# Kernel tuning notes

Hardware: AMD Instinct MI355X
Metric: run time of the kernel (lower is better)

Reference implementation:

```python
import jax, jax.numpy as jnp
import numpy as np


def setup_inputs() -> dict:
    key = jax.random.key(0)
    ks = jax.random.split(key, 6)
    B, H, W, Cin, Cout, wdim = 8, 64, 64, 512, 512, 512
    return {
        "x": jax.random.normal(ks[0], (B, H, W, Cin), jnp.float32),
        "w": jax.random.normal(ks[1], (B, wdim), jnp.float32),
        "noise": jax.random.normal(ks[2], (B, H, W, 1), jnp.float32),
        "style_weight": jax.random.normal(ks[3], (wdim, Cin), jnp.float32),
        "style_bias": jnp.ones((Cin,), jnp.float32),
        "conv_weight": jax.random.normal(ks[4], (3, 3, Cin, Cout), jnp.float32),
        "scale_noise": 0.1 * jax.random.normal(ks[5], (1, 1, 1, Cout), jnp.float32),
        "bias": jax.random.normal(jax.random.fold_in(key, 7), (Cout,), jnp.float32),
    }


def reference(x, w, noise, style_weight, style_bias, conv_weight, scale_noise, bias):
    wdim = style_weight.shape[0]
    kh, kw, cin, cout = conv_weight.shape
    # Equalized-LR fully connected to_style (gain=1, lr_mult=1, bias init ones,
    # activation=True -> leaky_relu(0.2) with sqrt(2) gain, StyleGAN2 convention).
    s = w @ (style_weight * (1.0 / np.sqrt(wdim))) + style_bias  # [B, Cin]
    s = jax.nn.leaky_relu(s, 0.2) * np.sqrt(2.0).astype(np.float32)
    # Modulated conv (demodulated). Equalized-LR weight scale 1/sqrt(fan_in).
    wk = conv_weight * (1.0 / np.sqrt(kh * kw * cin))  # [3,3,Cin,Cout]
    # demod[b,o] = rsqrt(sum_{h,w,i} (wk[h,w,i,o]*s[b,i])^2 + eps)
    d = jax.lax.rsqrt(jnp.einsum('hwio,bi->bo', wk * wk, s * s) + 1e-8)  # [B,Cout]
    xm = x * s[:, None, None, :]  # modulate inputs instead of per-sample weights
    y = jax.lax.conv_general_dilated(
        xm, wk, window_strides=(1, 1), padding='SAME',
        dimension_numbers=('NHWC', 'HWIO', 'NHWC'))
    y = y * d[:, None, None, :]
    # noise scale-add + bias + leaky-relu (the fused tail in StyleGAN2 kernels)
    y = y + scale_noise * noise + bias
    return jax.nn.leaky_relu(y, 0.2)
```

## Files before the change

kernel.cpp:

```cpp
#include <hip/hip_runtime.h>
#include <hip/hip_bf16.h>
#include <stdint.h>


typedef __attribute__((ext_vector_type(8))) __bf16 bf16x8;
typedef __attribute__((ext_vector_type(16))) float f32x16;

__device__ __forceinline__ float bf2f(ushort u) {
    union { uint32_t i; float f; } v; v.i = (uint32_t)u << 16; return v.f;
}
__device__ __forceinline__ ushort f2bf(float f) {
    union { float f; uint32_t i; } v; v.f = f;
    uint32_t r = v.i + 0x7fffu + ((v.i >> 16) & 1u);
    return (ushort)(r >> 16);
}
__device__ __forceinline__ int sniff_f32(const void* sb) {
    return ((const uint32_t*)sb)[0] == 0x3F800000u;
}
__device__ __forceinline__ float lda(const void* p, int idx, int isf) {
    return isf ? ((const float*)p)[idx] : bf2f(((const ushort*)p)[idx]);
}

union U16x8 { uint4 v; ushort u[8]; };

#define INV_SQRT_WDIM 0.04419417382415922f
#define SQRT2         1.4142135623730951f
#define WSCALE        0.014731391274719739f

__global__ void k_style_part(const void* __restrict__ w, const void* __restrict__ sw,
                             const void* __restrict__ sb, float* __restrict__ part) {
    int isf = sniff_f32(sb);
    int b = blockIdx.x >> 3, ds = blockIdx.x & 7;
    int i = threadIdx.x;
    __shared__ float wrow[64];
    if (i < 64) wrow[i] = lda(w, b * 512 + ds * 64 + i, isf);
    __syncthreads();
    float acc = 0.f;
    if (isf) {
        const float* p = (const float*)sw + (size_t)ds * 64 * 512;
#pragma unroll 8
        for (int d = 0; d < 64; ++d) acc += wrow[d] * p[d * 512 + i];
    } else {
        const ushort* p = (const ushort*)sw + (size_t)ds * 64 * 512;
#pragma unroll 8
        for (int d = 0; d < 64; ++d) acc += wrow[d] * bf2f(p[d * 512 + i]);
    }
    part[(b * 8 + ds) * 512 + i] = acc;
}

__device__ __forceinline__ float style_s(const float* __restrict__ spart,
                                         const void* __restrict__ sb,
                                         int b, int i, int isf) {
    float a = 0.f;
#pragma unroll
    for (int ds = 0; ds < 8; ++ds) a += spart[(b * 8 + ds) * 512 + i];
    float s = a * INV_SQRT_WDIM + lda(sb, i, isf);
    return (s > 0.f ? s : 0.2f * s) * SQRT2;
}

__global__ void k_prep(const void* __restrict__ cw, const void* __restrict__ x,
                       const float* __restrict__ spart, const void* __restrict__ sb,
                       ushort* __restrict__ wkt2, ushort* __restrict__ xmp2,
                       float* __restrict__ part) {
    int isf = sniff_f32(sb);
    int bid = blockIdx.x;
    int tid = threadIdx.x;
    __shared__ __align__(16) char pool[34816];

    if (bid < 576) {
        ushort (*smw)[512] = (ushort (*)[512])pool;
        int t = bid / 64, ckg = bid % 64;
#pragma unroll
        for (int r = 0; r < 16; ++r) {
            int l = r * 256 + tid;
            int j = l >> 9, o = l & 511;
            float v = lda(cw, (size_t)(t * 512 + ckg * 8 + j) * 512 + o, isf);
            smw[j][o] = f2bf(v * WSCALE);
        }
        __syncthreads();
#pragma unroll
        for (int r = 0; r < 2; ++r) {
            int o = r * 256 + tid;
            U16x8 pk;
#pragma unroll
            for (int j = 0; j < 8; ++j) pk.u[j] = smw[j][o];
            *(uint4*)(wkt2 + ((size_t)(t * 64 + ckg) * 512 + o) * 8) = pk.v;
        }
        return;
    }
    if (bid < 1104) {
        float* sv = (float*)pool;
        ushort* tr = (ushort*)(pool + 2048);
        int pr = bid - 576;
        int b = pr / 66, yp = pr % 66;
        ushort* xb2 = xmp2 + (size_t)b * 2230272;
        uint4 z = {0u, 0u, 0u, 0u};
        if (yp == 0 || yp == 65) {
            for (int l = tid; l < 4224; l += 256) {
                int h = l / 132, cc = l - h * 132;
                *(uint4*)(xb2 + (size_t)(h * 66 + yp) * 1056 + cc * 8) = z;
            }
            return;
        }
        for (int i = tid; i < 512; i += 256) sv[i] = style_s(spart, sb, b, i, isf);
        if (tid < 64) {
            int h = tid & 31, side = tid >> 5;
            ushort* op = xb2 + ((size_t)(h * 66 + yp) * 66 + side * 65) * 16;
            *(uint4*)(op) = z;
            *(uint4*)(op + 8) = z;
        }
        int y = yp - 1;
        __syncthreads();
#pragma unroll 1
        for (int p = 0; p < 2; ++p) {
            if (p) __syncthreads();
            int c0 = p * 32;
#pragma unroll
            for (int r = 0; r < 4; ++r) {
                int u = r * 256 + tid;
                int hg = u & 31, col = u >> 5;
                U16x8 o0_, o1_;
                const float* sp = sv + hg * 16;
                if (isf) {
                    const float* xin = (const float*)x
                        + (((size_t)(b * 64 + y)) * 64 + c0 + col) * 512 + hg * 16;
                    float4 f0 = *(const float4*)(xin + 0);
                    float4 f1 = *(const float4*)(xin + 4);
                    float4 f2 = *(const float4*)(xin + 8);
                    float4 f3 = *(const float4*)(xin + 12);
                    o0_.u[0] = f2bf(f0.x * sp[0]);  o0_.u[1] = f2bf(f0.y * sp[1]);
                    o0_.u[2] = f2bf(f0.z * sp[2]);  o0_.u[3] = f2bf(f0.w * sp[3]);
                    o0_.u[4] = f2bf(f1.x * sp[4]);  o0_.u[5] = f2bf(f1.y * sp[5]);
                    o0_.u[6] = f2bf(f1.z * sp[6]);  o0_.u[7] = f2bf(f1.w * sp[7]);
                    o1_.u[0] = f2bf(f2.x * sp[8]);  o1_.u[1] = f2bf(f2.y * sp[9]);
                    o1_.u[2] = f2bf(f2.z * sp[10]); o1_.u[3] = f2bf(f2.w * sp[11]);
                    o1_.u[4] = f2bf(f3.x * sp[12]); o1_.u[5] = f2bf(f3.y * sp[13]);
                    o1_.u[6] = f2bf(f3.z * sp[14]); o1_.u[7] = f2bf(f3.w * sp[15]);
                } else {
                    const ushort* xin = (const ushort*)x
                        + (((size_t)(b * 64 + y)) * 64 + c0 + col) * 512 + hg * 16;
                    U16x8 i0, i1;
                    i0.v = *(const uint4*)(xin);
                    i1.v = *(const uint4*)(xin + 8);
#pragma unroll
                    for (int j = 0; j < 8; ++j) o0_.u[j] = f2bf(bf2f(i0.u[j]) * sp[j]);
#pragma unroll
                    for (int j = 0; j < 8; ++j) o1_.u[j] = f2bf(bf2f(i1.u[j]) * sp[8 + j]);
                }
                int cs = col ^ (hg & 7);
                *(uint4*)(tr + ((hg * 2 + 0) * 32 + cs) * 8) = o0_.v;
                *(uint4*)(tr + ((hg * 2 + 1) * 32 + cs) * 8) = o1_.v;
            }
            __syncthreads();
#pragma unroll
            for (int r = 0; r < 4; ++r) {
                int v = r * 256 + tid;
                int col = v & 31, hg = v >> 5;
                int cs = col ^ (hg & 7);
                uint4 a0 = *(const uint4*)(tr + ((hg * 2 + 0) * 32 + cs) * 8);
                uint4 a1 = *(const uint4*)(tr + ((hg * 2 + 1) * 32 + cs) * 8);
                ushort* op = xb2 + ((size_t)(hg * 66 + yp) * 66 + (c0 + col + 1)) * 16;
                *(uint4*)(op) = a0;
                *(uint4*)(op + 8) = a1;
            }
        }
        return;
    }
    {
        float* s2 = (float*)pool;
        float* red = (float*)(pool + 16384);
        int q2 = bid - 1104;
        int t = q2 / 8, ob = q2 % 8;
#pragma unroll
        for (int j = 0; j < 16; ++j) {
            int idx = j * 256 + tid;
            int bb = idx >> 9, i = idx & 511;
            float scv = style_s(spart, sb, bb, i, isf);
            s2[idx] = scv * scv;
        }
        __syncthreads();
        int q = tid >> 6, ol = tid & 63;
        int o = ob * 64 + ol;
        float accd[8] = {0, 0, 0, 0, 0, 0, 0, 0};
        for (int ii = 0; ii < 128; ++ii) {
            int i = q * 128 + ii;
            float wf = lda(cw, (size_t)(t * 512 + i) * 512 + o, isf) * WSCALE;
            float w2 = wf * wf;
#pragma unroll
            for (int bb = 0; bb < 8; ++bb) accd[bb] += w2 * s2[bb * 512 + i];
        }
#pragma unroll
        for (int bb = 0; bb < 8; ++bb) red[(ol * 8 + bb) * 4 + q] = accd[bb];
        __syncthreads();
#pragma unroll
        for (int p = 0; p < 2; ++p) {
            int u = tid * 2 + p;
            int ol2 = u >> 3, b2 = u & 7;
            float sum = red[u * 4 + 0] + red[u * 4 + 1] + red[u * 4 + 2] + red[u * 4 + 3];
            part[(b2 * 9 + t) * 512 + ob * 64 + ol2] = sum;
        }
    }
}

#define GLL(gp, lp) __builtin_amdgcn_global_load_lds( \
    (const __attribute__((address_space(1))) void*)(gp), \
    (__attribute__((address_space(3))) void*)(lp), 16, 0, 0)

__launch_bounds__(256, 4)
__global__ void k_conv(const ushort* __restrict__ xmp2, const ushort* __restrict__ wkt2,
                       const float* __restrict__ part, const void* __restrict__ noise,
                       const void* __restrict__ snoise, const void* __restrict__ bias_,
                       const void* __restrict__ sb, void* __restrict__ out) {
    __shared__ ushort Ah[2][4224];
    int isf = sniff_f32(sb);
    int id = blockIdx.x;
    int ct = id & 3;
    int rt = (id >> 2) & 31;
    int b  = id >> 7;
    int y0 = rt * 2, o0 = ct * 128;
    int tid = threadIdx.x;
    int lane = tid & 63, wv = tid >> 6;
    int wr = wv >> 1, wc = wv & 1;
    int lm = lane & 31, kh = lane >> 5;
    const ushort* xb2 = xmp2 + (size_t)b * 2230272;
    const ushort* wB = wkt2 + kh * 4096 + (size_t)(o0 + wc * 64 + lm) * 8;

    auto stageA = [&](int hp, int buf) {
        char* dst = (char*)Ah[buf];
#pragma unroll
        for (int it = 0; it < 2; ++it) {
            int L = it * 256 + tid;
            int ck2 = L / 264, rem = L - ck2 * 264;
            int hr = rem / 66, col = rem - hr * 66;
            GLL(xb2 + (size_t)(hp * 66 + y0 + hr) * 1056 + col * 16 + ck2 * 8,
                dst + L * 16);
        }
        if (tid < 16) {
            int L = 512 + tid;
            int col = L - 264 - 198;
            GLL(xb2 + (size_t)(hp * 66 + y0 + 3) * 1056 + col * 16 + 8,
                dst + L * 16);
        }
    };
    auto loadB = [&](int t, int h, bf16x8 (&d)[2]) {
        const ushort* p = wB + (size_t)t * 262144 + h * 8192;
        d[0] = *(const bf16x8*)(p);
        d[1] = *(const bf16x8*)(p + 256);
    };

    f32x16 acc[2][2] = {};
    bf16x8 b0[2], b1[2], b2[2];

    stageA(0, 0);
    loadB(0, 0, b0);
    loadB(1, 0, b1);
    loadB(2, 0, b2);
    __syncthreads();

#pragma unroll 1
    for (int h = 0; h < 32; ++h) {
        const char* AhC = (const char*)Ah[h & 1];
        auto tap = [&](int t, const bf16x8 (&bf)[2]) {
            int dy = t / 3 - 1, dx = t % 3 - 1;
            bf16x8 afr[2];
#pragma unroll
            for (int am = 0; am < 2; ++am)
                afr[am] = *(const bf16x8*)(AhC
                    + (kh * 264
                       + (wr + dy + 1) * 66
                       + (am * 32 + lm + dx + 1)) * 16);
#pragma unroll
            for (int am = 0; am < 2; ++am)
#pragma unroll
                for (int bn = 0; bn < 2; ++bn)
                    acc[am][bn] = __builtin_amdgcn_mfma_f32_32x32x16_bf16(
                        afr[am], bf[bn], acc[am][bn], 0, 0, 0);
        };
        tap(0, b0); loadB(3, h, b0);
        if (h < 31) stageA(h + 1, (h + 1) & 1);
        tap(1, b1); loadB(4, h, b1);
        tap(2, b2); loadB(5, h, b2);
        tap(3, b0); loadB(6, h, b0);
        tap(4, b1); loadB(7, h, b1);
        tap(5, b2); loadB(8, h, b2);
        tap(6, b0); if (h < 31) loadB(0, h + 1, b0);
        tap(7, b1); if (h < 31) loadB(1, h + 1, b1);
        tap(8, b2); if (h < 31) loadB(2, h + 1, b2);
        if (h < 31) __syncthreads();
    }

    float dv[2], snv[2], bv[2];
#pragma unroll
    for (int bn = 0; bn < 2; ++bn) {
        int o = o0 + wc * 64 + bn * 32 + lm;
        float a = 1e-8f;
#pragma unroll
        for (int t = 0; t < 9; ++t) a += part[(b * 9 + t) * 512 + o];
        dv[bn] = rsqrtf(a);
        snv[bn] = lda(snoise, o, isf);
        bv[bn] = lda(bias_, o, isf);
    }
#pragma unroll
    for (int am = 0; am < 2; ++am) {
#pragma unroll
        for (int reg = 0; reg < 16; ++reg) {
            int crow = 4 * kh + (reg & 3) + 8 * (reg >> 2);
            int yy = y0 + wr;
            int xx = am * 32 + crow;
            float nz = lda(noise, (b * 64 + yy) * 64 + xx, isf);
            size_t obase = ((size_t)(b * 64 + yy) * 64 + xx) * 512;
            if (isf) {
                float* of = (float*)out;
#pragma unroll
                for (int bn = 0; bn < 2; ++bn) {
                    float v = acc[am][bn][reg] * dv[bn] + snv[bn] * nz + bv[bn];
                    v = v > 0.f ? v : 0.2f * v;
                    of[obase + o0 + wc * 64 + bn * 32 + lm] = v;
                }
            } else {
                ushort* ob = (ushort*)out;
#pragma unroll
                for (int bn = 0; bn < 2; ++bn) {
                    float v = acc[am][bn][reg] * dv[bn] + snv[bn] * nz + bv[bn];
                    v = v > 0.f ? v : 0.2f * v;
                    ob[obase + o0 + wc * 64 + bn * 32 + lm] = f2bf(v);
                }
            }
        }
    }
}

extern "C" void kernel_launch(void* const* d_in, const int* in_sizes, int n_in,
                              void* d_out, int out_size, void* d_ws, size_t ws_size,
                              hipStream_t stream) {
    const void* x     = d_in[0];
    const void* w     = d_in[1];
    const void* noise = d_in[2];
    const void* sw    = d_in[3];
    const void* sb    = d_in[4];
    const void* cw    = d_in[5];
    const void* sn    = d_in[6];
    const void* bias  = d_in[7];

    char* ws = (char*)d_ws;
    ushort* xmp2  = (ushort*)(ws);
    ushort* wkt2  = (ushort*)(ws + 35684352);
    float*  part  = (float*)(ws + 40435712);
    float*  spart = (float*)(ws + 40583168);
    (void)in_sizes; (void)n_in; (void)out_size; (void)ws_size;

    hipLaunchKernelGGL(k_style_part, dim3(64),   dim3(512), 0, stream, w, sw, sb, spart);
    hipLaunchKernelGGL(k_prep,       dim3(1176), dim3(256), 0, stream,
                       cw, x, spart, sb, wkt2, xmp2, part);
    hipLaunchKernelGGL(k_conv,       dim3(1024), dim3(256), 0, stream,
                       xmp2, wkt2, part, noise, sn, bias, sb, d_out);
}
```

Baseline: 318.8 us.

## Fuse input modulation into conv A-staging and fold demod into weight prep

Removes the separate padded, modulated bf16 copy of x. The conv kernel now loads raw x through registers, multiplies by the style vector, converts to bf16 and writes it into LDS. This overlaps with the MFMA taps and replaces the async global-to-LDS loads. The demodulation sums are computed inside the weight-transpose blocks with atomicAdd into a buffer zeroed by the style kernel, which drops the dedicated demod blocks. It saves a full write and read of the modulated activation tensor, but conv must now read fp32 x, possibly several times because of halo rows. The register-staged conversion adds VGPR pressure and ALU work to the main loop.

```diff
diff --git a/kernel.cpp b/kernel.cpp
--- a/kernel.cpp
+++ b/kernel.cpp
@@ -28,10 +28,13 @@
 #define WSCALE        0.014731391274719739f
 
 __global__ void k_style_part(const void* __restrict__ w, const void* __restrict__ sw,
-                             const void* __restrict__ sb, float* __restrict__ part) {
+                             const void* __restrict__ sb, float* __restrict__ spart,
+                             float* __restrict__ dpart) {
     int isf = sniff_f32(sb);
     int b = blockIdx.x >> 3, ds = blockIdx.x & 7;
     int i = threadIdx.x;
+    int gid = blockIdx.x * 512 + i;
+    for (int u2 = gid; u2 < 8 * 9 * 512; u2 += 64 * 512) dpart[u2] = 0.f;
     __shared__ float wrow[64];
     if (i < 64) wrow[i] = lda(w, b * 512 + ds * 64 + i, isf);
     __syncthreads();
@@ -45,7 +48,7 @@
 #pragma unroll 8
         for (int d = 0; d < 64; ++d) acc += wrow[d] * bf2f(p[d * 512 + i]);
     }
-    part[(b * 8 + ds) * 512 + i] = acc;
+    spart[(b * 8 + ds) * 512 + i] = acc;
 }
 
 __device__ __forceinline__ float style_s(const float* __restrict__ spart,
@@ -58,160 +61,57 @@
     return (s > 0.f ? s : 0.2f * s) * SQRT2;
 }
 
-__global__ void k_prep(const void* __restrict__ cw, const void* __restrict__ x,
-                       const float* __restrict__ spart, const void* __restrict__ sb,
-                       ushort* __restrict__ wkt2, ushort* __restrict__ xmp2,
-                       float* __restrict__ part) {
+__global__ void k_prep2(const void* __restrict__ cw, const float* __restrict__ spart,
+                        const void* __restrict__ sb, ushort* __restrict__ wkt2,
+                        float* __restrict__ dpart) {
     int isf = sniff_f32(sb);
     int bid = blockIdx.x;
     int tid = threadIdx.x;
-    __shared__ __align__(16) char pool[34816];
-
-    if (bid < 576) {
-        ushort (*smw)[512] = (ushort (*)[512])pool;
-        int t = bid / 64, ckg = bid % 64;
-#pragma unroll
-        for (int r = 0; r < 16; ++r) {
-            int l = r * 256 + tid;
-            int j = l >> 9, o = l & 511;
-            float v = lda(cw, (size_t)(t * 512 + ckg * 8 + j) * 512 + o, isf);
-            smw[j][o] = f2bf(v * WSCALE);
-        }
-        __syncthreads();
-#pragma unroll
-        for (int r = 0; r < 2; ++r) {
-            int o = r * 256 + tid;
-            U16x8 pk;
-#pragma unroll
-            for (int j = 0; j < 8; ++j) pk.u[j] = smw[j][o];
-            *(uint4*)(wkt2 + ((size_t)(t * 64 + ckg) * 512 + o) * 8) = pk.v;
-        }
-        return;
-    }
-    if (bid < 1104) {
-        float* sv = (float*)pool;
-        ushort* tr = (ushort*)(pool + 2048);
-        int pr = bid - 576;
-        int b = pr / 66, yp = pr % 66;
-        ushort* xb2 = xmp2 + (size_t)b * 2230272;
-        uint4 z = {0u, 0u, 0u, 0u};
-        if (yp == 0 || yp == 65) {
-            for (int l = tid; l < 4224; l += 256) {
-                int h = l / 132, cc = l - h * 132;
-                *(uint4*)(xb2 + (size_t)(h * 66 + yp) * 1056 + cc * 8) = z;
-            }
-            return;
-        }
-        for (int i = tid; i < 512; i += 256) sv[i] = style_s(spart, sb, b, i, isf);
-        if (tid < 64) {
-            int h = tid & 31, side = tid >> 5;
-            ushort* op = xb2 + ((size_t)(h * 66 + yp) * 66 + side * 65) * 16;
-            *(uint4*)(op) = z;
-            *(uint4*)(op + 8) = z;
-        }
-        int y = yp - 1;
-        __syncthreads();
-#pragma unroll 1
-        for (int p = 0; p < 2; ++p) {
-            if (p) __syncthreads();
-            int c0 = p * 32;
-#pragma unroll
-            for (int r = 0; r < 4; ++r) {
-                int u = r * 256 + tid;
-                int hg = u & 31, col = u >> 5;
-                U16x8 o0_, o1_;
-                const float* sp = sv + hg * 16;
-                if (isf) {
-                    const float* xin = (const float*)x
-                        + (((size_t)(b * 64 + y)) * 64 + c0 + col) * 512 + hg * 16;
-                    float4 f0 = *(const float4*)(xin + 0);
-                    float4 f1 = *(const float4*)(xin + 4);
-                    float4 f2 = *(const float4*)(xin + 8);
-                    float4 f3 = *(const float4*)(xin + 12);
-                    o0_.u[0] = f2bf(f0.x * sp[0]);  o0_.u[1] = f2bf(f0.y * sp[1]);
-                    o0_.u[2] = f2bf(f0.z * sp[2]);  o0_.u[3] = f2bf(f0.w * sp[3]);
-                    o0_.u[4] = f2bf(f1.x * sp[4]);  o0_.u[5] = f2bf(f1.y * sp[5]);
-                    o0_.u[6] = f2bf(f1.z * sp[6]);  o0_.u[7] = f2bf(f1.w * sp[7]);
-                    o1_.u[0] = f2bf(f2.x * sp[8]);  o1_.u[1] = f2bf(f2.y * sp[9]);
-                    o1_.u[2] = f2bf(f2.z * sp[10]); o1_.u[3] = f2bf(f2.w * sp[11]);
-                    o1_.u[4] = f2bf(f3.x * sp[12]); o1_.u[5] = f2bf(f3.y * sp[13]);
-                    o1_.u[6] = f2bf(f3.z * sp[14]); o1_.u[7] = f2bf(f3.w * sp[15]);
-                } else {
-                    const ushort* xin = (const ushort*)x
-                        + (((size_t)(b * 64 + y)) * 64 + c0 + col) * 512 + hg * 16;
-                    U16x8 i0, i1;
-                    i0.v = *(const uint4*)(xin);
-                    i1.v = *(const uint4*)(xin + 8);
-#pragma unroll
-                    for (int j = 0; j < 8; ++j) o0_.u[j] = f2bf(bf2f(i0.u[j]) * sp[j]);
-#pragma unroll
-                    for (int j = 0; j < 8; ++j) o1_.u[j] = f2bf(bf2f(i1.u[j]) * sp[8 + j]);
-                }
-                int cs = col ^ (hg & 7);
-                *(uint4*)(tr + ((hg * 2 + 0) * 32 + cs) * 8) = o0_.v;
-                *(uint4*)(tr + ((hg * 2 + 1) * 32 + cs) * 8) = o1_.v;
-            }
-            __syncthreads();
-#pragma unroll
-            for (int r = 0; r < 4; ++r) {
-                int v = r * 256 + tid;
-                int col = v & 31, hg = v >> 5;
-                int cs = col ^ (hg & 7);
-                uint4 a0 = *(const uint4*)(tr + ((hg * 2 + 0) * 32 + cs) * 8);
-                uint4 a1 = *(const uint4*)(tr + ((hg * 2 + 1) * 32 + cs) * 8);
-                ushort* op = xb2 + ((size_t)(hg * 66 + yp) * 66 + (c0 + col + 1)) * 16;
-                *(uint4*)(op) = a0;
-                *(uint4*)(op + 8) = a1;
-            }
-        }
-        return;
-    }
-    {
-        float* s2 = (float*)pool;
-        float* red = (float*)(pool + 16384);
-        int q2 = bid - 1104;
-        int t = q2 / 8, ob = q2 % 8;
-#pragma unroll
-        for (int j = 0; j < 16; ++j) {
-            int idx = j * 256 + tid;
-            int bb = idx >> 9, i = idx & 511;
-            float scv = style_s(spart, sb, bb, i, isf);
-            s2[idx] = scv * scv;
-        }
-        __syncthreads();
-        int q = tid >> 6, ol = tid & 63;
-        int o = ob * 64 + ol;
-        float accd[8] = {0, 0, 0, 0, 0, 0, 0, 0};
-        for (int ii = 0; ii < 128; ++ii) {
-            int i = q * 128 + ii;
-            float wf = lda(cw, (size_t)(t * 512 + i) * 512 + o, isf) * WSCALE;
+    int t = bid / 64, ckg = bid % 64;
+    __shared__ ushort smw[8][512];
+    __shared__ float s2l[8][8];
+    if (tid < 64) {
+        int j = tid >> 3, b = tid & 7;
+        float v = style_s(spart, sb, b, ckg * 8 + j, isf);
+        s2l[j][b] = v * v;
+    }
+#pragma unroll
+    for (int r = 0; r < 16; ++r) {
+        int l = r * 256 + tid;
+        int j = l >> 9, o = l & 511;
+        float v = lda(cw, (size_t)(t * 512 + ckg * 8 + j) * 512 + o, isf);
+        smw[j][o] = f2bf(v * WSCALE);
+    }
+    __syncthreads();
+#pragma unroll
+    for (int r = 0; r < 2; ++r) {
+        int o = r * 256 + tid;
+        U16x8 pk;
+        float ds[8] = {0, 0, 0, 0, 0, 0, 0, 0};
+#pragma unroll
+        for (int j = 0; j < 8; ++j) {
+            ushort u = smw[j][o];
+            pk.u[j] = u;
+            float wf = bf2f(u);
             float w2 = wf * wf;
 #pragma unroll
-            for (int bb = 0; bb < 8; ++bb) accd[bb] += w2 * s2[bb * 512 + i];
-        }
-#pragma unroll
-        for (int bb = 0; bb < 8; ++bb) red[(ol * 8 + bb) * 4 + q] = accd[bb];
-        __syncthreads();
-#pragma unroll
-        for (int p = 0; p < 2; ++p) {
-            int u = tid * 2 + p;
-            int ol2 = u >> 3, b2 = u & 7;
-            float sum = red[u * 4 + 0] + red[u * 4 + 1] + red[u * 4 + 2] + red[u * 4 + 3];
-            part[(b2 * 9 + t) * 512 + ob * 64 + ol2] = sum;
-        }
-    }
-}
-
-#define GLL(gp, lp) __builtin_amdgcn_global_load_lds( \
-    (const __attribute__((address_space(1))) void*)(gp), \
-    (__attribute__((address_space(3))) void*)(lp), 16, 0, 0)
+            for (int b = 0; b < 8; ++b) ds[b] += w2 * s2l[j][b];
+        }
+        *(uint4*)(wkt2 + ((size_t)(t * 64 + ckg) * 512 + o) * 8) = pk.v;
+#pragma unroll
+        for (int b = 0; b < 8; ++b)
+            atomicAdd(&dpart[(b * 9 + t) * 512 + o], ds[b]);
+    }
+}
 
 __launch_bounds__(256, 4)
-__global__ void k_conv(const ushort* __restrict__ xmp2, const ushort* __restrict__ wkt2,
-                       const float* __restrict__ part, const void* __restrict__ noise,
-                       const void* __restrict__ snoise, const void* __restrict__ bias_,
-                       const void* __restrict__ sb, void* __restrict__ out) {
-    __shared__ ushort Ah[2][4224];
+__global__ void k_conv(const void* __restrict__ x, const ushort* __restrict__ wkt2,
+                       const float* __restrict__ dpart, const float* __restrict__ spart,
+                       const void* __restrict__ noise, const void* __restrict__ snoise,
+                       const void* __restrict__ bias_, const void* __restrict__ sb,
+                       void* __restrict__ out) {
+    __shared__ __align__(16) ushort Ah[2][4224];
+    __shared__ float sv[512];
     int isf = sniff_f32(sb);
     int id = blockIdx.x;
     int ct = id & 3;
@@ -222,36 +122,75 @@
     int lane = tid & 63, wv = tid >> 6;
     int wr = wv >> 1, wc = wv & 1;
     int lm = lane & 31, kh = lane >> 5;
-    const ushort* xb2 = xmp2 + (size_t)b * 2230272;
+    int qt = tid & 3;
     const ushort* wB = wkt2 + kh * 4096 + (size_t)(o0 + wc * 64 + lm) * 8;
 
-    auto stageA = [&](int hp, int buf) {
-        char* dst = (char*)Ah[buf];
-#pragma unroll
-        for (int it = 0; it < 2; ++it) {
-            int L = it * 256 + tid;
-            int ck2 = L / 264, rem = L - ck2 * 264;
-            int hr = rem / 66, col = rem - hr * 66;
-            GLL(xb2 + (size_t)(hp * 66 + y0 + hr) * 1056 + col * 16 + ck2 * 8,
-                dst + L * 16);
-        }
-        if (tid < 16) {
-            int L = 512 + tid;
-            int col = L - 264 - 198;
-            GLL(xb2 + (size_t)(hp * 66 + y0 + 3) * 1056 + col * 16 + 8,
-                dst + L * 16);
-        }
-    };
     auto loadB = [&](int t, int h, bf16x8 (&d)[2]) {
         const ushort* p = wB + (size_t)t * 262144 + h * 8192;
         d[0] = *(const bf16x8*)(p);
         d[1] = *(const bf16x8*)(p + 256);
     };
 
+    float4 xf[4];
+    uint4  xb[4];
+    auto issueX = [&](int hp) {
+#pragma unroll
+        for (int r = 0; r < 4; ++r) {
+            int cell = r * 64 + (tid >> 2);
+            int row = cell >> 6, px = cell & 63;
+            int y = y0 + row - 1;
+            if ((unsigned)y < 64u) {
+                if (isf) {
+                    xf[r] = *(const float4*)((const float*)x
+                        + (((size_t)(b * 64 + y)) * 64 + px) * 512 + hp * 16 + qt * 4);
+                } else if (qt < 2) {
+                    xb[r] = *(const uint4*)((const ushort*)x
+                        + (((size_t)(b * 64 + y)) * 64 + px) * 512 + hp * 16 + qt * 8);
+                }
+            }
+        }
+    };
+    auto writeX = [&](int hp, int buf) {
+        char* dst = (char*)Ah[buf];
+#pragma unroll
+        for (int r = 0; r < 4; ++r) {
+            int cell = r * 64 + (tid >> 2);
+            int row = cell >> 6, px = cell & 63;
+            int y = y0 + row - 1;
+            if ((unsigned)y < 64u) {
+                if (isf) {
+                    const float* sp = sv + hp * 16 + qt * 4;
+                    ushort4 o4;
+                    o4.x = f2bf(xf[r].x * sp[0]);
+                    o4.y = f2bf(xf[r].y * sp[1]);
+                    o4.z = f2bf(xf[r].z * sp[2]);
+                    o4.w = f2bf(xf[r].w * sp[3]);
+                    *(ushort4*)(dst + ((qt >> 1) * 264 + row * 66 + px + 1) * 16
+                                    + (qt & 1) * 8) = o4;
+                } else if (qt < 2) {
+                    const float* sp = sv + hp * 16 + qt * 8;
+                    U16x8 in, o8;
+                    in.v = xb[r];
+#pragma unroll
+                    for (int j = 0; j < 8; ++j) o8.u[j] = f2bf(bf2f(in.u[j]) * sp[j]);
+                    *(uint4*)(dst + (qt * 264 + row * 66 + px + 1) * 16) = o8.v;
+                }
+            }
+        }
+    };
+
     f32x16 acc[2][2] = {};
     bf16x8 b0[2], b1[2], b2[2];
 
-    stageA(0, 0);
+    issueX(0);
+    {
+        uint4 z4 = {0u, 0u, 0u, 0u};
+        uint4* za = (uint4*)Ah;
+        for (int l = tid; l < 1056; l += 256) za[l] = z4;
+        for (int c = tid; c < 512; c += 256) sv[c] = style_s(spart, sb, b, c, isf);
+    }
+    __syncthreads();
+    writeX(0, 0);
     loadB(0, 0, b0);
     loadB(1, 0, b1);
     loadB(2, 0, b2);
@@ -260,6 +199,7 @@
 #pragma unroll 1
     for (int h = 0; h < 32; ++h) {
         const char* AhC = (const char*)Ah[h & 1];
+        if (h < 31) issueX(h + 1);
         auto tap = [&](int t, const bf16x8 (&bf)[2]) {
             int dy = t / 3 - 1, dx = t % 3 - 1;
             bf16x8 afr[2];
@@ -277,9 +217,9 @@
                         afr[am], bf[bn], acc[am][bn], 0, 0, 0);
         };
         tap(0, b0); loadB(3, h, b0);
-        if (h < 31) stageA(h + 1, (h + 1) & 1);
         tap(1, b1); loadB(4, h, b1);
         tap(2, b2); loadB(5, h, b2);
+        if (h < 31) writeX(h + 1, (h + 1) & 1);
         tap(3, b0); loadB(6, h, b0);
         tap(4, b1); loadB(7, h, b1);
         tap(5, b2); loadB(8, h, b2);
@@ -295,7 +235,7 @@
         int o = o0 + wc * 64 + bn * 32 + lm;
         float a = 1e-8f;
 #pragma unroll
-        for (int t = 0; t < 9; ++t) a += part[(b * 9 + t) * 512 + o];
+        for (int t = 0; t < 9; ++t) a += dpart[(b * 9 + t) * 512 + o];
         dv[bn] = rsqrtf(a);
         snv[bn] = lda(snoise, o, isf);
         bv[bn] = lda(bias_, o, isf);
@@ -343,15 +283,15 @@
     const void* bias  = d_in[7];
 
     char* ws = (char*)d_ws;
-    ushort* xmp2  = (ushort*)(ws);
-    ushort* wkt2  = (ushort*)(ws + 35684352);
-    float*  part  = (float*)(ws + 40435712);
-    float*  spart = (float*)(ws + 40583168);
+    ushort* wkt2  = (ushort*)(ws);
+    float*  dpart = (float*)(ws + 4718592);
+    float*  spart = (float*)(ws + 4866048);
     (void)in_sizes; (void)n_in; (void)out_size; (void)ws_size;
 
-    hipLaunchKernelGGL(k_style_part, dim3(64),   dim3(512), 0, stream, w, sw, sb, spart);
-    hipLaunchKernelGGL(k_prep,       dim3(1176), dim3(256), 0, stream,
-                       cw, x, spart, sb, wkt2, xmp2, part);
+    hipLaunchKernelGGL(k_style_part, dim3(64),   dim3(512), 0, stream,
+                       w, sw, sb, spart, dpart);
+    hipLaunchKernelGGL(k_prep2,      dim3(576),  dim3(256), 0, stream,
+                       cw, spart, sb, wkt2, dpart);
     hipLaunchKernelGGL(k_conv,       dim3(1024), dim3(256), 0, stream,
-                       xmp2, wkt2, part, noise, sn, bias, sb, d_out);
-}
+                       x, wkt2, dpart, spart, noise, sn, bias, sb, d_out);
+}
```

After: 468.1 us. 46.8% more time.
